# Kernel tuning notes

Measured on AMD Instinct MI355X. Metric: run time of the kernel, lower is better.

The kernel has to match this reference:

```python
import jax, jax.numpy as jnp
import numpy as np

# --- fixed hyperparameters (from module source / standard iSTFTNet config) ---
D_MODEL = 256      # h.upsample_initial_channel (must be 256 to match conv_post in_channels)
D_STATE = 64
D_CONV = 4
EXPAND = 2
D_INNER = EXPAND * D_MODEL          # 512
DT_RANK = D_MODEL // 16             # 16 (ceil(d_model/16))
N_FFT = 16                          # h.gen_istft_n_fft
BATCH, MELS, SEQ = 4, 80, 2048
LEAKY_SLOPE = 0.01


def conv1d(x, w, b, pad):
    # x: [B, Cin, L], w: [Cout, Cin, K] -> [B, Cout, L]
    y = jax.lax.conv_general_dilated(x, w, window_strides=(1,), padding=[(pad, pad)],
                                     dimension_numbers=('NCH', 'OIH', 'NCH'))
    return y + b[None, :, None]


def setup_inputs() -> dict:
    key = jax.random.key(0)
    ks = jax.random.split(key, 16)
    s = 0.02
    inp = {
        'x':           jax.random.normal(ks[0], (BATCH, MELS, SEQ), jnp.float32),
        # conv_pre: Conv1d(80, 256, 7, padding=3); weight-norm is a reparam, use effective weight
        'conv_pre_w':  jax.random.normal(ks[1], (D_MODEL, MELS, 7), jnp.float32) * 0.01,
        'conv_pre_b':  jax.random.normal(ks[2], (D_MODEL,), jnp.float32) * s,
        # Mamba params
        'in_proj_w':   jax.random.normal(ks[3], (2 * D_INNER, D_MODEL), jnp.float32) * s,
        'dw_conv_w':   jax.random.normal(ks[4], (D_INNER, 1, D_CONV), jnp.float32) * s,   # depthwise causal
        'dw_conv_b':   jax.random.normal(ks[5], (D_INNER,), jnp.float32) * s,
        'x_proj_w':    jax.random.normal(ks[6], (DT_RANK + 2 * D_STATE, D_INNER), jnp.float32) * s,
        'dt_proj_w':   jax.random.normal(ks[7], (D_INNER, DT_RANK), jnp.float32) * s,
        'dt_proj_b':   jax.random.normal(ks[8], (D_INNER,), jnp.float32) * s,
        # S4D-real init: A = -exp(A_log), A_log = log(1..d_state) broadcast over d_inner
        'A_log':       jnp.broadcast_to(jnp.log(jnp.arange(1, D_STATE + 1, dtype=jnp.float32)),
                                        (D_INNER, D_STATE)).copy(),
        'D_skip':      jnp.ones((D_INNER,), jnp.float32),
        'out_proj_w':  jax.random.normal(ks[9], (D_MODEL, D_INNER), jnp.float32) * s,
        # conv_post: Conv1d(256, n_fft+2=18, 7, padding=3)
        'conv_post_w': jax.random.normal(ks[10], (N_FFT + 2, D_MODEL, 7), jnp.float32) * 0.01,
        'conv_post_b': jax.random.normal(ks[11], (N_FFT + 2,), jnp.float32) * s,
    }
    return inp


def reference(x, conv_pre_w, conv_pre_b, in_proj_w, dw_conv_w, dw_conv_b,
              x_proj_w, dt_proj_w, dt_proj_b, A_log, D_skip, out_proj_w,
              conv_post_w, conv_post_b):
    # conv_pre: [B, 80, L] -> [B, 256, L]
    h = conv1d(x, conv_pre_w, conv_pre_b, pad=3)
    ht = h.transpose(0, 2, 1)                          # [B, L, 256]

    # --- Mamba block ---
    xz = ht @ in_proj_w.T                              # [B, L, 2*d_inner]
    u, z = jnp.split(xz, 2, axis=-1)                   # each [B, L, d_inner]

    # causal depthwise conv over time (left pad d_conv-1), then SiLU
    uc = u.transpose(0, 2, 1)                          # [B, d_inner, L]
    uc = jax.lax.conv_general_dilated(uc, dw_conv_w, window_strides=(1,),
                                      padding=[(D_CONV - 1, 0)],
                                      dimension_numbers=('NCH', 'OIH', 'NCH'),
                                      feature_group_count=D_INNER)
    uc = jax.nn.silu(uc + dw_conv_b[None, :, None])
    u = uc.transpose(0, 2, 1)                          # [B, L, d_inner]

    x_dbl = u @ x_proj_w.T                             # [B, L, dt_rank + 2*N]
    dt = x_dbl[..., :DT_RANK]
    Bc = x_dbl[..., DT_RANK:DT_RANK + D_STATE]         # [B, L, N]
    Cc = x_dbl[..., DT_RANK + D_STATE:]                # [B, L, N]
    delta = jax.nn.softplus(dt @ dt_proj_w.T + dt_proj_b)  # [B, L, d_inner]

    A = -jnp.exp(A_log)                                # [d_inner, N]

    def step(hstate, inp):
        d_t, B_t, C_t, u_t = inp                       # [B,d], [B,N], [B,N], [B,d]
        dA = jnp.exp(d_t[..., None] * A)               # [B, d, N]
        hstate = dA * hstate + (d_t * u_t)[..., None] * B_t[:, None, :]
        y_t = jnp.einsum('bdn,bn->bd', hstate, C_t)
        return hstate, y_t

    xs = (delta.transpose(1, 0, 2), Bc.transpose(1, 0, 2),
          Cc.transpose(1, 0, 2), u.transpose(1, 0, 2))
    h0 = jnp.zeros((x.shape[0], D_INNER, D_STATE), dtype=x.dtype)
    _, ys = jax.lax.scan(step, h0, xs)                 # ys: [L, B, d_inner]
    y = ys.transpose(1, 0, 2) + u * D_skip             # skip connection D*u
    y = y * jax.nn.silu(z)                             # gate
    out = y @ out_proj_w.T                             # [B, L, 256]

    # back to [B, C, L], leaky_relu, conv_post
    oc = out.transpose(0, 2, 1)
    oc = jnp.where(oc >= 0, oc, LEAKY_SLOPE * oc)
    oc = conv1d(oc, conv_post_w, conv_post_b, pad=3)   # [B, 18, L]

    half = N_FFT // 2 + 1                              # 9
    spec = jnp.exp(oc[:, :half, :])
    phase = jnp.sin(oc[:, half:, :])
    return spec, phase
```

## Files before the change

### kernel.cpp

```cpp
#include <hip/hip_runtime.h>
#include <cstdint>

#define DEV __device__ __forceinline__

DEV float sigmoidf_(float x){ return 1.f / (1.f + __expf(-x)); }
DEV float siluf_(float x){ return x * sigmoidf_(x); }
DEV float softplusf_(float x){ return x > 20.f ? x : log1pf(__expf(x)); }
DEV float lreluf_(float x){ return x >= 0.f ? x : 0.01f * x; }

DEV unsigned short f2bf(float f){
    union { float f; uint32_t u; } v; v.f = f;
    uint32_t u = v.u;
    u += 0x7fffu + ((u >> 16) & 1u);
    return (unsigned short)(u >> 16);
}

#define L2E 1.4426950408889634f

typedef __attribute__((ext_vector_type(8))) short bf16x8;
typedef __attribute__((ext_vector_type(4))) float f32x4;

__global__ __launch_bounds__(256) void k_conv_pre(const float* __restrict__ x,
    const float* __restrict__ w, const float* __restrict__ bias,
    unsigned short* __restrict__ h_bf)
{
    const int b = blockIdx.y;
    const int t0 = blockIdx.x * 16;
    const int c = threadIdx.x;
    __shared__ float sX[80][22];
    for (int idx = threadIdx.x; idx < 80 * 22; idx += 256) {
        int m = idx / 22, tt = idx - m * 22;
        int ta = t0 - 3 + tt;
        sX[m][tt] = (ta >= 0 && ta < 2048) ? x[(b * 80 + m) * 2048 + ta] : 0.f;
    }
    __syncthreads();
    float acc[16];
    float bv = bias[c];
    #pragma unroll
    for (int i = 0; i < 16; i++) acc[i] = bv;
    const float* wrow = w + c * 560;
    for (int m = 0; m < 80; ++m) {
        float xr[22];
        #pragma unroll
        for (int q = 0; q < 22; q++) xr[q] = sX[m][q];
        #pragma unroll
        for (int k = 0; k < 7; k++) {
            float wv = wrow[m * 7 + k];
            #pragma unroll
            for (int tt = 0; tt < 16; tt++) acc[tt] = fmaf(xr[k + tt], wv, acc[tt]);
        }
    }
    for (int tt = 0; tt < 16; tt++)
        h_bf[(b * 2048 + t0 + tt) * 256 + c] = f2bf(acc[tt]);
}

__global__ void k_pack3(const float* __restrict__ s0, int n0,
                        const float* __restrict__ s1, int n1,
                        const float* __restrict__ s2, int n2,
                        unsigned short* __restrict__ dst)
{
    int i = blockIdx.x * 256 + threadIdx.x;
    int j = i;
    const float* s;
    if (j < n0) s = s0;
    else if ((j -= n0) < n1) s = s1;
    else { j -= n1; if (j >= n2) return; s = s2; }
    dst[i] = f2bf(s[j]);
}

template<int PERM>
__global__ __launch_bounds__(256) void k_gemm_mfma(const unsigned short* __restrict__ A,
    const unsigned short* __restrict__ B, float* __restrict__ C, int M, int N, int K)
{
    __shared__ unsigned short As[64][72];
    __shared__ unsigned short Bs[64][72];
    const int tid = threadIdx.x;
    const int bm = blockIdx.y * 64, bn = blockIdx.x * 64;
    const int w = tid >> 6, lane = tid & 63;
    const int l16 = lane & 15, quad = lane >> 4;
    const int lrow = tid >> 3, lcol = tid & 7;
    f32x4 acc[4] = {};
    for (int k0 = 0; k0 < K; k0 += 64) {
        __syncthreads();
        #pragma unroll
        for (int hh = 0; hh < 2; ++hh) {
            int r = lrow + 32 * hh;
            *(uint4*)&As[r][lcol * 8] = *(const uint4*)(A + (size_t)(bm + r) * K + k0 + lcol * 8);
            uint4 bvv = make_uint4(0, 0, 0, 0);
            if (bn + r < N) bvv = *(const uint4*)(B + (size_t)(bn + r) * K + k0 + lcol * 8);
            *(uint4*)&Bs[r][lcol * 8] = bvv;
        }
        __syncthreads();
        #pragma unroll
        for (int kk = 0; kk < 64; kk += 32) {
            bf16x8 af = *(const bf16x8*)&As[w * 16 + l16][kk + quad * 8];
            #pragma unroll
            for (int nt = 0; nt < 4; ++nt) {
                bf16x8 bfr = *(const bf16x8*)&Bs[nt * 16 + l16][kk + quad * 8];
                acc[nt] = __builtin_amdgcn_mfma_f32_16x16x32_bf16(af, bfr, acc[nt], 0, 0, 0);
            }
        }
    }
    #pragma unroll
    for (int nt = 0; nt < 4; ++nt) {
        #pragma unroll
        for (int i = 0; i < 4; ++i) {
            int m = bm + w * 16 + quad * 4 + i;
            int n = bn + nt * 16 + l16;
            if (n < N) {
                int nn = n;
                if (PERM) nn = (n < 16) ? n : (n < 80 ? 16 + 2 * (n - 16) : 17 + 2 * (n - 80));
                C[(size_t)m * N + nn] = acc[nt][i];
            }
        }
    }
}

template<int ACT, int PERM>
__global__ __launch_bounds__(256) void k_gemm_nt(const float* __restrict__ A,
    const float* __restrict__ B, const float* __restrict__ bias, float* __restrict__ C,
    int M, int N, int K, int lda, int ldb)
{
    __shared__ float As[16][64];
    __shared__ float Bs[16][64];
    const int bm = blockIdx.y * 64, bn = blockIdx.x * 64;
    const int tid = threadIdx.x;
    const int lm = tid >> 2, lk = (tid & 3) * 4;
    const int tx = tid & 15, ty = tid >> 4;
    float acc[4][4];
    #pragma unroll
    for (int i = 0; i < 4; i++)
        #pragma unroll
        for (int j = 0; j < 4; j++) acc[i][j] = 0.f;
    for (int k0 = 0; k0 < K; k0 += 16) {
        float4 av = make_float4(0.f,0.f,0.f,0.f), bv = make_float4(0.f,0.f,0.f,0.f);
        if (bm + lm < M) av = *(const float4*)(A + (size_t)(bm + lm) * lda + k0 + lk);
        if (bn + lm < N) bv = *(const float4*)(B + (size_t)(bn + lm) * ldb + k0 + lk);
        __syncthreads();
        As[lk + 0][lm] = av.x; As[lk + 1][lm] = av.y; As[lk + 2][lm] = av.z; As[lk + 3][lm] = av.w;
        Bs[lk + 0][lm] = bv.x; Bs[lk + 1][lm] = bv.y; Bs[lk + 2][lm] = bv.z; Bs[lk + 3][lm] = bv.w;
        __syncthreads();
        #pragma unroll
        for (int kk = 0; kk < 16; kk++) {
            float4 a  = *(const float4*)&As[kk][ty * 4];
            float4 b4 = *(const float4*)&Bs[kk][tx * 4];
            acc[0][0] = fmaf(a.x, b4.x, acc[0][0]); acc[0][1] = fmaf(a.x, b4.y, acc[0][1]);
            acc[0][2] = fmaf(a.x, b4.z, acc[0][2]); acc[0][3] = fmaf(a.x, b4.w, acc[0][3]);
            acc[1][0] = fmaf(a.y, b4.x, acc[1][0]); acc[1][1] = fmaf(a.y, b4.y, acc[1][1]);
            acc[1][2] = fmaf(a.y, b4.z, acc[1][2]); acc[1][3] = fmaf(a.y, b4.w, acc[1][3]);
            acc[2][0] = fmaf(a.z, b4.x, acc[2][0]); acc[2][1] = fmaf(a.z, b4.y, acc[2][1]);
            acc[2][2] = fmaf(a.z, b4.z, acc[2][2]); acc[2][3] = fmaf(a.z, b4.w, acc[2][3]);
            acc[3][0] = fmaf(a.w, b4.x, acc[3][0]); acc[3][1] = fmaf(a.w, b4.y, acc[3][1]);
            acc[3][2] = fmaf(a.w, b4.z, acc[3][2]); acc[3][3] = fmaf(a.w, b4.w, acc[3][3]);
        }
    }
    #pragma unroll
    for (int i = 0; i < 4; i++) {
        int m = bm + ty * 4 + i;
        if (m >= M) continue;
        #pragma unroll
        for (int j = 0; j < 4; j++) {
            int n = bn + tx * 4 + j;
            if (n >= N) continue;
            float v = acc[i][j];
            if (bias) v += bias[n];
            if (ACT == 1) v = softplusf_(v);
            int nn = n;
            if (PERM) nn = (n < 16) ? n : (n < 80 ? 16 + 2 * (n - 16) : 17 + 2 * (n - 80));
            C[(size_t)m * N + nn] = v;
        }
    }
}

__global__ __launch_bounds__(256) void k_dwconv(const float* __restrict__ xz,
    const float* __restrict__ w, const float* __restrict__ bias,
    float* __restrict__ uc, unsigned short* __restrict__ uc_bf)
{
    int idx = blockIdx.x * 256 + threadIdx.x;
    int i = idx >> 9, d = idx & 511;
    int b = i >> 11, t = i & 2047;
    float4 wv = *(const float4*)(w + d * 4);
    float wk[4] = {wv.x, wv.y, wv.z, wv.w};
    float acc = bias[d];
    const float* base = xz + (size_t)(b * 2048) * 1024 + d;
    #pragma unroll
    for (int k = 0; k < 4; k++) {
        int tt = t - 3 + k;
        if (tt >= 0) acc = fmaf(base[(size_t)tt * 1024], wk[k], acc);
    }
    float s = siluf_(acc);
    uc[idx] = s;
    uc_bf[idx] = f2bf(s);
}

#define DECAY_LADDER(e, rbase, r)                                     \
    {                                                                 \
        e[0] = rbase; e[1] = rbase * r;                               \
        float r2_ = r * r;                                            \
        e[2] = e[0] * r2_; e[3] = e[1] * r2_;                         \
        float r4_ = r2_ * r2_;                                        \
        _Pragma("unroll")                                             \
        for (int j_ = 0; j_ < 4; ++j_) e[4 + j_] = e[j_] * r4_;       \
        float r8_ = r4_ * r4_;                                        \
        _Pragma("unroll")                                             \
        for (int j_ = 0; j_ < 8; ++j_) e[8 + j_] = e[j_] * r8_;       \
        float r16_ = r8_ * r8_;                                       \
        _Pragma("unroll")                                             \
        for (int j_ = 0; j_ < 16; ++j_) e[16 + j_] = e[j_] * r16_;    \
    }

__global__ __launch_bounds__(256, 4) void k_scan1(const float* __restrict__ delta,
    const float* __restrict__ uc, const float* __restrict__ xdbl,
    const float* __restrict__ A_log, float* __restrict__ hloc, float* __restrict__ sumdg)
{
    __shared__ float sBC[32 * 128];
    const int tid = threadIdx.x;
    const int c = blockIdx.x, dg = blockIdx.y, b = blockIdx.z;
    const int w = tid >> 6, lane = tid & 63;
    const int dl5 = lane & 31, half = lane >> 5;
    const int d = dg * 128 + w * 32 + dl5;
    const int nbase = half * 32;
    for (int idx = tid; idx < 1024; idx += 256) {
        int r = idx >> 5, q = idx & 31;
        *(float4*)&sBC[r * 128 + q * 4] =
            *(const float4*)(xdbl + (size_t)(b * 2048 + c * 32 + r) * 144 + 16 + q * 4);
    }
    const float A2base = -__expf(A_log[(size_t)d * 64 + nbase]) * L2E;
    float h[32];
    #pragma unroll
    for (int n = 0; n < 32; ++n) h[n] = 0.f;
    __syncthreads();
    const float* pD = delta + (size_t)(b * 2048 + c * 32) * 512 + d;
    const float* pU = uc    + (size_t)(b * 2048 + c * 32) * 512 + d;
    float sumd = 0.f;
    for (int t = 0; t < 32; ++t) {
        float dl = pD[(size_t)t * 512];
        float u  = pU[(size_t)t * 512];
        float du = dl * u;
        sumd += dl;
        float rbase = exp2f(dl * A2base);
        float r     = exp2f(-dl * L2E);
        float e[32];
        DECAY_LADDER(e, rbase, r);
        const float* bct = &sBC[t * 128 + half * 64];
        #pragma unroll
        for (int n = 0; n < 32; n += 2) {
            float4 bc = *(const float4*)(bct + 2 * n);
            h[n]     = fmaf(e[n],     h[n],     du * bc.x);
            h[n + 1] = fmaf(e[n + 1], h[n + 1], du * bc.z);
        }
    }
    float* hp = hloc + ((size_t)c * 2048 + b * 512 + d) * 64 + nbase;
    #pragma unroll
    for (int n = 0; n < 32; n += 4)
        *(float4*)(hp + n) = make_float4(h[n], h[n + 1], h[n + 2], h[n + 3]);
    if (half == 0)
        sumdg[(size_t)c * 2048 + b * 512 + d] = sumd;
}

__global__ __launch_bounds__(256) void k_carry(float* __restrict__ hloc,
    const float* __restrict__ sumdg, const float* __restrict__ A_log)
{
    int tid = blockIdx.x * 256 + threadIdx.x;
    int bd = tid >> 6, n = tid & 63, d = bd & 511;
    float A2 = -__expf(A_log[d * 64 + n]) * L2E;
    float carry = hloc[tid];
    for (int cc = 1; cc < 63; ++cc) {
        float P = exp2f(sumdg[(size_t)cc * 2048 + bd] * A2);
        size_t o = (size_t)cc * 131072 + tid;
        carry = fmaf(carry, P, hloc[o]);
        hloc[o] = carry;
    }
}

__global__ __launch_bounds__(256, 4) void k_scan2f(const float* __restrict__ delta,
    const float* __restrict__ uc, const float* __restrict__ xz,
    const float* __restrict__ xdbl, const float* __restrict__ A_log,
    const float* __restrict__ hcar, const float* __restrict__ Dskip,
    unsigned short* __restrict__ g_bf)
{
    __shared__ float sBC[32 * 128];
    const int tid = threadIdx.x;
    const int c = blockIdx.x, dg = blockIdx.y, b = blockIdx.z;
    const int w = tid >> 6, lane = tid & 63;
    const int dl5 = lane & 31, half = lane >> 5;
    const int d = dg * 128 + w * 32 + dl5;
    const int nbase = half * 32;
    for (int idx = tid; idx < 1024; idx += 256) {
        int r = idx >> 5, q = idx & 31;
        *(float4*)&sBC[r * 128 + q * 4] =
            *(const float4*)(xdbl + (size_t)(b * 2048 + c * 32 + r) * 144 + 16 + q * 4);
    }
    const float A2base = -__expf(A_log[(size_t)d * 64 + nbase]) * L2E;
    float h[32];
    if (c == 0) {
        #pragma unroll
        for (int n = 0; n < 32; ++n) h[n] = 0.f;
    } else {
        const float* hp = hcar + ((size_t)(c - 1) * 2048 + b * 512 + d) * 64 + nbase;
        #pragma unroll
        for (int k = 0; k < 8; ++k) {
            float4 hv = *(const float4*)(hp + k * 4);
            h[4 * k + 0] = hv.x; h[4 * k + 1] = hv.y;
            h[4 * k + 2] = hv.z; h[4 * k + 3] = hv.w;
        }
    }
    __syncthreads();
    const float dsk = Dskip[d];
    for (int t = 0; t < 32; ++t) {
        size_t R = (size_t)(b * 2048 + c * 32 + t);
        float dl = delta[R * 512 + d];
        float u  = uc[R * 512 + d];
        float z  = xz[R * 1024 + 512 + d];
        float du = dl * u;
        float rbase = exp2f(dl * A2base);
        float r     = exp2f(-dl * L2E);
        float e[32];
        DECAY_LADDER(e, rbase, r);
        const float* bct = &sBC[t * 128 + half * 64];
        float y0 = 0.f, y1 = 0.f;
        #pragma unroll
        for (int n = 0; n < 32; n += 2) {
            float4 bc = *(const float4*)(bct + 2 * n);
            h[n] = fmaf(e[n], h[n], du * bc.x);
            y0 = fmaf(h[n], bc.y, y0);
            h[n + 1] = fmaf(e[n + 1], h[n + 1], du * bc.z);
            y1 = fmaf(h[n + 1], bc.w, y1);
        }
        float yh = y0 + y1;
        yh += __shfl_xor(yh, 32, 64);
        if (half == 0) {
            float y = yh + u * dsk;
            g_bf[R * 512 + d] = f2bf(y * siluf_(z));
        }
    }
}

__global__ void k_transpose_wpost(const float* __restrict__ w, float* __restrict__ wT)
{
    int idx = blockIdx.x * 256 + threadIdx.x;
    if (idx >= 18 * 256 * 7) return;
    int o = idx / 1792, rem = idx - o * 1792;
    int c = rem / 7, k = rem - c * 7;
    wT[k * 4608 + o * 256 + c] = w[idx];
}

__global__ __launch_bounds__(320) void k_conv_post(const float* __restrict__ mid,
    const float* __restrict__ wT, const float* __restrict__ bias, float* __restrict__ out)
{
    __shared__ float sX[22][260];
    const int tid = threadIdx.x;
    const int b = blockIdx.y, t0 = blockIdx.x * 16;
    for (int idx = tid; idx < 22 * 256; idx += 320) {
        int r = idx >> 8, c = idx & 255;
        int ta = t0 - 3 + r;
        float v = 0.f;
        if (ta >= 0 && ta < 2048) v = lreluf_(mid[(size_t)(b * 2048 + ta) * 256 + c]);
        sX[r][c] = v;
    }
    __syncthreads();
    const int t = tid & 15, o = tid >> 4;
    if (o >= 18) return;
    float a0 = 0.f, a1 = 0.f, a2 = 0.f, a3 = 0.f;
    for (int k = 0; k < 7; ++k) {
        const float* xr = &sX[t + k][0];
        const float* wr = wT + k * 4608 + o * 256;
        #pragma unroll 8
        for (int c = 0; c < 256; c += 4) {
            float4 xv = *(const float4*)(xr + c);
            float4 wv = *(const float4*)(wr + c);
            a0 = fmaf(xv.x, wv.x, a0); a1 = fmaf(xv.y, wv.y, a1);
            a2 = fmaf(xv.z, wv.z, a2); a3 = fmaf(xv.w, wv.w, a3);
        }
    }
    float v = (a0 + a1) + (a2 + a3) + bias[o];
    int ta = t0 + t;
    if (o < 9) out[(size_t)(b * 9 + o) * 2048 + ta] = __expf(v);
    else       out[73728 + (size_t)(b * 9 + (o - 9)) * 2048 + ta] = __sinf(v);
}

extern "C" void kernel_launch(void* const* d_in, const int* in_sizes, int n_in,
                              void* d_out, int out_size, void* d_ws, size_t ws_size,
                              hipStream_t stream)
{
    const float* x         = (const float*)d_in[0];
    const float* pre_w     = (const float*)d_in[1];
    const float* pre_b     = (const float*)d_in[2];
    const float* inproj_w  = (const float*)d_in[3];
    const float* dw_w      = (const float*)d_in[4];
    const float* dw_b      = (const float*)d_in[5];
    const float* xproj_w   = (const float*)d_in[6];
    const float* dt_w      = (const float*)d_in[7];
    const float* dt_b      = (const float*)d_in[8];
    const float* A_log     = (const float*)d_in[9];
    const float* Dskip     = (const float*)d_in[10];
    const float* outproj_w = (const float*)d_in[11];
    const float* post_w    = (const float*)d_in[12];
    const float* post_b    = (const float*)d_in[13];
    float* out = (float*)d_out;
    float* W = (float*)d_ws;

    float* xz      = W;
    float* uc      = W + 8388608;
    float* x_dbl   = W + 12582912;
    float* delta   = W + 13762560;
    float* hloc    = W + 17956864;
    float* sumd    = W + 26214400;
    float* wTpost  = W + 26343424;
    unsigned short* h_bf  = (unsigned short*)(W + 26375680);
    unsigned short* uc_bf = (unsigned short*)(W + 27424256);
    unsigned short* g_bf  = (unsigned short*)(W + 29521408);
    unsigned short* wbf_i = (unsigned short*)(W + 31618560);
    unsigned short* wbf_x = wbf_i + 262144;
    unsigned short* wbf_o = wbf_x + 73728;
    float* out_mid = hloc;

    k_pack3<<<1824, 256, 0, stream>>>(inproj_w, 262144, xproj_w, 73728,
                                      outproj_w, 131072, wbf_i);
    k_conv_pre<<<dim3(128, 4), 256, 0, stream>>>(x, pre_w, pre_b, h_bf);
    k_gemm_mfma<0><<<dim3(16, 128), 256, 0, stream>>>(h_bf, wbf_i, xz, 8192, 1024, 256);
    k_dwconv<<<16384, 256, 0, stream>>>(xz, dw_w, dw_b, uc, uc_bf);
    k_gemm_mfma<1><<<dim3(3, 128), 256, 0, stream>>>(uc_bf, wbf_x, x_dbl, 8192, 144, 512);
    k_gemm_nt<1,0><<<dim3(8, 128), 256, 0, stream>>>(x_dbl, dt_w, dt_b, delta,
                                                     8192, 512, 16, 144, 16);
    k_scan1<<<dim3(63, 4, 4), 256, 0, stream>>>(delta, uc, x_dbl, A_log, hloc, sumd);
    k_carry<<<512, 256, 0, stream>>>(hloc, sumd, A_log);
    k_scan2f<<<dim3(64, 4, 4), 256, 0, stream>>>(delta, uc, xz, x_dbl, A_log,
                                                 hloc, Dskip, g_bf);
    k_gemm_mfma<0><<<dim3(4, 128), 256, 0, stream>>>(g_bf, wbf_o, out_mid, 8192, 256, 512);
    k_transpose_wpost<<<126, 256, 0, stream>>>(post_w, wTpost);
    k_conv_post<<<dim3(128, 4), 320, 0, stream>>>(out_mid, wTpost, post_b, out);
}
```

Before: 369.1 us.

## Convert conv_pre to im2col plus bf16 MFMA GEMM with fused bias

Replaces the scalar FP32 conv_pre kernel with an im2col pass that builds a bf16 [8192 x 576] patch matrix, a packed bf16 weight matrix, and a call to the existing MFMA GEMM. The GEMM gains bias and bf16-output options so the conv result goes straight into h_bf. This moves the roughly 2.3 GFLOP pre-convolution onto matrix cores, at the cost of two extra launches and writing and reading about 9 MB of im2col data. It also reduces the input and weight precision of this conv to bf16.

```diff
diff --git a/kernel.cpp b/kernel.cpp
--- a/kernel.cpp
+++ b/kernel.cpp
@@ -19,40 +19,6 @@
 
 typedef __attribute__((ext_vector_type(8))) short bf16x8;
 typedef __attribute__((ext_vector_type(4))) float f32x4;
-
-__global__ __launch_bounds__(256) void k_conv_pre(const float* __restrict__ x,
-    const float* __restrict__ w, const float* __restrict__ bias,
-    unsigned short* __restrict__ h_bf)
-{
-    const int b = blockIdx.y;
-    const int t0 = blockIdx.x * 16;
-    const int c = threadIdx.x;
-    __shared__ float sX[80][22];
-    for (int idx = threadIdx.x; idx < 80 * 22; idx += 256) {
-        int m = idx / 22, tt = idx - m * 22;
-        int ta = t0 - 3 + tt;
-        sX[m][tt] = (ta >= 0 && ta < 2048) ? x[(b * 80 + m) * 2048 + ta] : 0.f;
-    }
-    __syncthreads();
-    float acc[16];
-    float bv = bias[c];
-    #pragma unroll
-    for (int i = 0; i < 16; i++) acc[i] = bv;
-    const float* wrow = w + c * 560;
-    for (int m = 0; m < 80; ++m) {
-        float xr[22];
-        #pragma unroll
-        for (int q = 0; q < 22; q++) xr[q] = sX[m][q];
-        #pragma unroll
-        for (int k = 0; k < 7; k++) {
-            float wv = wrow[m * 7 + k];
-            #pragma unroll
-            for (int tt = 0; tt < 16; tt++) acc[tt] = fmaf(xr[k + tt], wv, acc[tt]);
-        }
-    }
-    for (int tt = 0; tt < 16; tt++)
-        h_bf[(b * 2048 + t0 + tt) * 256 + c] = f2bf(acc[tt]);
-}
 
 __global__ void k_pack3(const float* __restrict__ s0, int n0,
                         const float* __restrict__ s1, int n1,
@@ -68,9 +34,32 @@
     dst[i] = f2bf(s[j]);
 }
 
-template<int PERM>
+__global__ void k_pack_prew(const float* __restrict__ w, unsigned short* __restrict__ dst)
+{
+    int i = blockIdx.x * 256 + threadIdx.x;
+    if (i >= 256 * 576) return;
+    int r = i / 576, c = i - r * 576;
+    dst[i] = (c < 560) ? f2bf(w[r * 560 + c]) : (unsigned short)0;
+}
+
+__global__ void k_im2col(const float* __restrict__ x, unsigned short* __restrict__ A)
+{
+    int i = blockIdx.x * 256 + threadIdx.x;
+    int row = i / 576, col = i - row * 576;
+    int b = row >> 11, t = row & 2047;
+    unsigned short v = 0;
+    if (col < 560) {
+        int m = col / 7, k = col - m * 7;
+        int ta = t - 3 + k;
+        if (ta >= 0 && ta < 2048) v = f2bf(x[(b * 80 + m) * 2048 + ta]);
+    }
+    A[i] = v;
+}
+
+template<int PERM, int OUTBF>
 __global__ __launch_bounds__(256) void k_gemm_mfma(const unsigned short* __restrict__ A,
-    const unsigned short* __restrict__ B, float* __restrict__ C, int M, int N, int K)
+    const unsigned short* __restrict__ B, const float* __restrict__ bias,
+    void* __restrict__ Cv, int M, int N, int K)
 {
     __shared__ unsigned short As[64][72];
     __shared__ unsigned short Bs[64][72];
@@ -103,15 +92,17 @@
     }
     #pragma unroll
     for (int nt = 0; nt < 4; ++nt) {
+        int n = bn + nt * 16 + l16;
+        if (n >= N) continue;
+        float bv = bias ? bias[n] : 0.f;
+        int nn = n;
+        if (PERM) nn = (n < 16) ? n : (n < 80 ? 16 + 2 * (n - 16) : 17 + 2 * (n - 80));
         #pragma unroll
         for (int i = 0; i < 4; ++i) {
             int m = bm + w * 16 + quad * 4 + i;
-            int n = bn + nt * 16 + l16;
-            if (n < N) {
-                int nn = n;
-                if (PERM) nn = (n < 16) ? n : (n < 80 ? 16 + 2 * (n - 16) : 17 + 2 * (n - 80));
-                C[(size_t)m * N + nn] = acc[nt][i];
-            }
+            float v = acc[nt][i] + bv;
+            if (OUTBF) ((unsigned short*)Cv)[(size_t)m * N + nn] = f2bf(v);
+            else       ((float*)Cv)[(size_t)m * N + nn] = v;
         }
     }
 }
@@ -413,21 +404,29 @@
     unsigned short* wbf_i = (unsigned short*)(W + 31618560);
     unsigned short* wbf_x = wbf_i + 262144;
     unsigned short* wbf_o = wbf_x + 73728;
+    unsigned short* wbf_p = wbf_o + 131072;
+    unsigned short* A_bf  = (unsigned short*)hloc;
     float* out_mid = hloc;
 
     k_pack3<<<1824, 256, 0, stream>>>(inproj_w, 262144, xproj_w, 73728,
                                       outproj_w, 131072, wbf_i);
-    k_conv_pre<<<dim3(128, 4), 256, 0, stream>>>(x, pre_w, pre_b, h_bf);
-    k_gemm_mfma<0><<<dim3(16, 128), 256, 0, stream>>>(h_bf, wbf_i, xz, 8192, 1024, 256);
+    k_pack_prew<<<576, 256, 0, stream>>>(pre_w, wbf_p);
+    k_im2col<<<18432, 256, 0, stream>>>(x, A_bf);
+    k_gemm_mfma<0,1><<<dim3(4, 128), 256, 0, stream>>>(A_bf, wbf_p, pre_b,
+                                                       h_bf, 8192, 256, 576);
+    k_gemm_mfma<0,0><<<dim3(16, 128), 256, 0, stream>>>(h_bf, wbf_i, nullptr,
+                                                        xz, 8192, 1024, 256);
     k_dwconv<<<16384, 256, 0, stream>>>(xz, dw_w, dw_b, uc, uc_bf);
-    k_gemm_mfma<1><<<dim3(3, 128), 256, 0, stream>>>(uc_bf, wbf_x, x_dbl, 8192, 144, 512);
+    k_gemm_mfma<1,0><<<dim3(3, 128), 256, 0, stream>>>(uc_bf, wbf_x, nullptr,
+                                                       x_dbl, 8192, 144, 512);
     k_gemm_nt<1,0><<<dim3(8, 128), 256, 0, stream>>>(x_dbl, dt_w, dt_b, delta,
                                                      8192, 512, 16, 144, 16);
     k_scan1<<<dim3(63, 4, 4), 256, 0, stream>>>(delta, uc, x_dbl, A_log, hloc, sumd);
     k_carry<<<512, 256, 0, stream>>>(hloc, sumd, A_log);
     k_scan2f<<<dim3(64, 4, 4), 256, 0, stream>>>(delta, uc, xz, x_dbl, A_log,
                                                  hloc, Dskip, g_bf);
-    k_gemm_mfma<0><<<dim3(4, 128), 256, 0, stream>>>(g_bf, wbf_o, out_mid, 8192, 256, 512);
+    k_gemm_mfma<0,0><<<dim3(4, 128), 256, 0, stream>>>(g_bf, wbf_o, nullptr,
+                                                       out_mid, 8192, 256, 512);
     k_transpose_wpost<<<126, 256, 0, stream>>>(post_w, wTpost);
     k_conv_post<<<dim3(128, 4), 320, 0, stream>>>(out_mid, wTpost, post_b, out);
 }
```

After: 349.5 us. 5.3% less time.
